# Performance work log

Measured on AMD Instinct MI355X. Metric: run time of the kernel, lower is better.

Reference implementation:

```python
import jax, jax.numpy as jnp
import numpy as np
from jax import lax

K = 5  # SCNN_KERNEL_LENGTH
PAD = K - 1
PAD_L = PAD // 2
PAD_R = PAD - PAD_L


def setup_inputs() -> dict:
    key = jax.random.key(0)
    k1, k2 = jax.random.split(key)
    B, H, W, C = 16, 256, 256, 32
    inputs = jax.random.normal(k1, (B, H, W, C), dtype=jnp.float32)
    # keras 'random_uniform' init is small; scale randn similarly to keep relu chain stable
    w = jax.random.normal(k2, (C, K, 1, C), dtype=jnp.float32) * 0.05
    b = jnp.zeros((C,), dtype=jnp.float32)
    return {"inputs": inputs, "w": w, "b": b}


def _mvcnn_down(inputs, w, b):
    # inputs: [B,H,W,C]; w: [C,K,1,C] (tf filter: [fh=C, fw=K, in=1, out=C])
    # The tf conv of the transposed row [B,C,W,1] with this filter is exactly a
    # 1D conv over W mixing all C input channels:
    #   out[b,x,o] = sum_{k,c} row_pad[b, x+k, c] * w[c,k,0,o]
    kernel = jnp.transpose(w[:, :, 0, :], (1, 0, 2))  # [K, C_in, C_out]

    def conv_row(x):  # x: [B,W,C] -> [B,W,C]
        return lax.conv_general_dilated(
            x, kernel, window_strides=(1,), padding=[(PAD_L, PAD_R)],
            dimension_numbers=("NWC", "WIO", "NWC"))

    rows = jnp.transpose(inputs, (1, 0, 2, 3))  # [H,B,W,C]

    def step(carry, row):
        # row i of the evolving state = original row + relu-conv result of row i-1
        x = row + carry
        r = jax.nn.relu(conv_row(x) + b)
        return r, r

    init = jnp.zeros_like(rows[0])
    _, out_rows = lax.scan(step, init, rows)  # [H,B,W,C]
    return jnp.transpose(out_rows, (1, 0, 2, 3))  # [B,H,W,C]


def reference(inputs, w, b):
    return _mvcnn_down(inputs, w, b)
```

## Files before the change

### kernel.cpp

```cpp
#include <hip/hip_runtime.h>
#include <stdint.h>

typedef _Float16 f16;
typedef _Float16 f16x2 __attribute__((ext_vector_type(2)));
typedef _Float16 f16x8 __attribute__((ext_vector_type(8)));
typedef float f32x4 __attribute__((ext_vector_type(4)));

#define NB 16
#define NH 256
#define NW 256
#define NC 32
#define NK 5

#define OWN 16
#define GC 16
#define NBLK (NB * GC)
#define XSTR 40
#define XROWS 36

#define FLAG_U32 16
#define NSLOT (NBLK * 2 * 2)
#define NFLAGS (NSLOT * FLAG_U32)
#define MAIL_BASE NFLAGS
#define MAIL_WORDS 128
#define KEYOF(k) (0x5EED0000u ^ (uint32_t)(k))

__device__ __forceinline__ void lds_barrier() {
  asm volatile("s_waitcnt lgkmcnt(0)\n\ts_barrier" ::: "memory");
}

__global__ __launch_bounds__(128, 1)
void mvcnn_down_mb(const float* __restrict__ in, const float* __restrict__ wt,
                   const float* __restrict__ bias, float* __restrict__ out,
                   uint32_t* __restrict__ ws) {
  __shared__ __align__(16) f16 xpad[2][XROWS * XSTR];

  const int bid  = blockIdx.x;
  const int b    = bid & 15;
  const int ck   = bid >> 4;
  const int t    = threadIdx.x;
  const int lane = t & 63;
  const int wv   = t >> 6;
  const int n16  = lane & 15;
  const int q    = lane >> 4;

  f16x8 bfrag[NK][2];
  #pragma unroll
  for (int tap = 0; tap < NK; ++tap) {
    #pragma unroll
    for (int nt = 0; nt < 2; ++nt) {
      f16x8 f;
      #pragma unroll
      for (int j = 0; j < 8; ++j) {
        int cch = q * 4 + (j >> 1) + (j & 1) * 16;
        f[j] = (f16)wt[(cch * NK + tap) * NC + nt * 16 + n16];
      }
      bfrag[tap][nt] = f;
    }
  }
  const float bias0 = bias[n16];
  const float bias1 = bias[16 + n16];

  for (int i = t; i < (int)(2 * XROWS * XSTR / 2); i += 128)
    ((uint32_t*)&xpad[0][0])[i] = 0u;

  const float* inb  = in  + (size_t)b * NH * NW * NC;
  float*       outb = out + (size_t)b * NH * NW * NC;

  const int lc0   = wv * 16 + q * 4;
  const int gcol0 = ck * 16 - 8 + lc0;

  int boff[4];
  #pragma unroll
  for (int r = 0; r < 4; ++r) {
    int g  = gcol0 + r;
    int gc = g < 0 ? 0 : (g > NW - 1 ? NW - 1 : g);
    boff[r] = (gc * NC + n16) * 4;
  }
  const bool ostore = wv ? (q < 2) : (q >= 2);
  const int  gown0  = wv ? (ck * 16 + 8 + q * 4) : (ck * 16 + (q - 2) * 4);

  uint32_t* flags = ws;
  uint32_t* mail  = ws + MAIL_BASE;
  const bool haspeer = wv ? (ck < GC - 1) : (ck > 0);
  const int  myslot2 = (bid * 2 + wv) * 2;
  const int  nbslot2 = wv ? ((bid + 16) * 2 + 0) * 2
                          : ((bid - 16) * 2 + 1) * 2;
  const int  smi     = wv ? (q * 4) * 16 : ((q - 2) * 4) * 16;

  float pf0[8], pf1[8];
  auto load_row = [&](int h1, float (&pf)[8]) {
    if (h1 >= NH) return;
    const char* rp = (const char*)(inb + (size_t)h1 * NW * NC);
    #pragma unroll
    for (int r = 0; r < 4; ++r) {
      pf[2 * r]     = *(const float*)(rp + boff[r]);
      pf[2 * r + 1] = *(const float*)(rp + boff[r] + 64);
    }
  };

  #pragma unroll
  for (int r = 0; r < 4; ++r) {
    int g = gcol0 + r;
    if ((unsigned)g < NW) {
      f16x2 v;
      v[0] = (f16)inb[g * NC + n16];
      v[1] = (f16)inb[g * NC + 16 + n16];
      *(f16x2*)(&xpad[0][(lc0 + r + 2) * XSTR + 2 * n16]) = v;
    }
  }
  load_row(1, pf0);
  load_row(2, pf1);
  __syncthreads();

  auto body = [&](const int h, float (&pf)[8], f16* xc, f16* xn,
                  bool recv, bool send) {
    if (recv) {
      const int k = h >> 2, ms = k & 1;
      if (haspeer) {
        if (lane == 0) {
          while (__hip_atomic_load(&flags[(nbslot2 + ms) * FLAG_U32],
                                   __ATOMIC_RELAXED, __HIP_MEMORY_SCOPE_AGENT)
                 != KEYOF(k))
            __builtin_amdgcn_s_sleep(2);
        }
        asm volatile("" ::: "memory");
        if (q < 2) {
          const uint32_t* mb = mail + (size_t)(nbslot2 + ms) * MAIL_WORDS;
          #pragma unroll
          for (int r = 0; r < 4; ++r) {
            uint32_t u = __hip_atomic_load(&mb[(q * 4 + r) * 16 + n16],
                                           __ATOMIC_RELAXED,
                                           __HIP_MEMORY_SCOPE_AGENT);
            const int lc = (wv ? 24 : 0) + q * 4 + r;
            *(uint32_t*)(&xc[(lc + 2) * XSTR + 2 * n16]) = u;
          }
        }
      }
    }

    f32x4 acc0 = {bias0, bias0, bias0, bias0};
    f32x4 acc1 = {bias1, bias1, bias1, bias1};
    #pragma unroll
    for (int tap = 0; tap < NK; ++tap) {
      f16x8 af = *(const f16x8*)(xc + (wv * 16 + n16 + tap) * XSTR + q * 8);
      acc0 = __builtin_amdgcn_mfma_f32_16x16x32_f16(af, bfrag[tap][0], acc0, 0, 0, 0);
      acc1 = __builtin_amdgcn_mfma_f32_16x16x32_f16(af, bfrag[tap][1], acc1, 0, 0, 0);
    }

    uint32_t sb[4] = {0, 0, 0, 0};
    float y0v[4], y1v[4];
    #pragma unroll
    for (int r = 0; r < 4; ++r) {
      float y0 = fmaxf(acc0[r], 0.f);
      float y1 = fmaxf(acc1[r], 0.f);
      y0v[r] = y0; y1v[r] = y1;
      int g = gcol0 + r;
      if (h < NH - 1 && (unsigned)g < NW) {
        f16x2 v;
        v[0] = (f16)(pf[2 * r]     + y0);
        v[1] = (f16)(pf[2 * r + 1] + y1);
        *(f16x2*)(&xn[(lc0 + r + 2) * XSTR + 2 * n16]) = v;
        sb[r] = __builtin_bit_cast(uint32_t, v);
      }
    }

    if (send && (h + 1) < NH) {
      const int k = (h + 1) >> 2, ms = k & 1;
      if (haspeer) {
        if (ostore) {
          uint32_t* mb = mail + (size_t)(myslot2 + ms) * MAIL_WORDS;
          #pragma unroll
          for (int r = 0; r < 4; ++r)
            __hip_atomic_store(&mb[smi + r * 16 + n16], sb[r],
                               __ATOMIC_RELAXED, __HIP_MEMORY_SCOPE_AGENT);
        }
        asm volatile("s_waitcnt vmcnt(0)" ::: "memory");
        if (lane == 0)
          __hip_atomic_store(&flags[(myslot2 + ms) * FLAG_U32], KEYOF(k),
                             __ATOMIC_RELAXED, __HIP_MEMORY_SCOPE_AGENT);
      }
    }

    if (ostore) {
      float* orow = outb + (size_t)h * NW * NC;
      #pragma unroll
      for (int r = 0; r < 4; ++r) {
        orow[(gown0 + r) * NC + n16]      = y0v[r];
        orow[(gown0 + r) * NC + 16 + n16] = y1v[r];
      }
    }

    load_row(h + 3, pf);
    lds_barrier();
  };

  f16* B0 = &xpad[0][0];
  f16* B1 = &xpad[1][0];
  for (int h4 = 0; h4 < NH; h4 += 4) {
    body(h4,     pf0, B0, B1, h4 > 0, false);
    body(h4 + 1, pf1, B1, B0, false,  false);
    body(h4 + 2, pf0, B0, B1, false,  false);
    body(h4 + 3, pf1, B1, B0, false,  true);
  }
}

__global__ __launch_bounds__(1024, 4)
void mvcnn_down(const float* __restrict__ in, const float* __restrict__ wt,
                const float* __restrict__ bias, float* __restrict__ out) {
  __shared__ __align__(16) f16 xpad[2][260 * XSTR];

  const int b    = blockIdx.x;
  const int t    = threadIdx.x;
  const int lane = t & 63;
  const int wv   = t >> 6;
  const int n16  = lane & 15;
  const int q    = lane >> 4;

  f16x8 bfrag[NK][2];
  #pragma unroll
  for (int tap = 0; tap < NK; ++tap) {
    #pragma unroll
    for (int nt = 0; nt < 2; ++nt) {
      f16x8 f;
      #pragma unroll
      for (int j = 0; j < 8; ++j) {
        int cch = q * 4 + (j >> 1) + (j & 1) * 16;
        f[j] = (f16)wt[(cch * NK + tap) * NC + nt * 16 + n16];
      }
      bfrag[tap][nt] = f;
    }
  }
  const float bias0 = bias[n16];
  const float bias1 = bias[16 + n16];

  for (int i = t; i < 2 * 260 * XSTR; i += 1024) (&xpad[0][0])[i] = (f16)0.f;
  __syncthreads();

  const float* inb  = in  + (size_t)b * NH * NW * NC;
  float*       outb = out + (size_t)b * NH * NW * NC;

  const int wo0  = wv * 16 + q * 4;
  const int arow = wv * 16 + n16;

  float pf0[8], pf1[8];
  auto load_in_row = [&](int h1, float (&pf)[8]) {
    const float* rp = inb + (size_t)h1 * NW * NC;
    #pragma unroll
    for (int r = 0; r < 4; ++r) {
      int wo = wo0 + r;
      pf[2 * r]     = rp[wo * NC + n16];
      pf[2 * r + 1] = rp[wo * NC + 16 + n16];
    }
  };

  #pragma unroll
  for (int r = 0; r < 4; ++r) {
    int wo = wo0 + r;
    f16x2 v;
    v[0] = (f16)inb[wo * NC + n16];
    v[1] = (f16)inb[wo * NC + 16 + n16];
    *(f16x2*)(&xpad[0][(wo + 2) * XSTR + 2 * n16]) = v;
  }
  load_in_row(1, pf0);
  load_in_row(2, pf1);
  __syncthreads();

  auto body = [&](const int h, float (&pf)[8], const f16* xp_cur, f16* xp_nxt) {
    f32x4 acc0 = {0.f, 0.f, 0.f, 0.f};
    f32x4 acc1 = {0.f, 0.f, 0.f, 0.f};
    #pragma unroll
    for (int tap = 0; tap < NK; ++tap) {
      f16x8 af = *(const f16x8*)(xp_cur + (arow + tap) * XSTR + q * 8);
      acc0 = __builtin_amdgcn_mfma_f32_16x16x32_f16(af, bfrag[tap][0], acc0, 0, 0, 0);
      acc1 = __builtin_amdgcn_mfma_f32_16x16x32_f16(af, bfrag[tap][1], acc1, 0, 0, 0);
    }
    float* orow = outb + (size_t)h * NW * NC;
    #pragma unroll
    for (int r = 0; r < 4; ++r) {
      float y0 = acc0[r] + bias0; y0 = y0 > 0.f ? y0 : 0.f;
      float y1 = acc1[r] + bias1; y1 = y1 > 0.f ? y1 : 0.f;
      int wo = wo0 + r;
      orow[wo * NC + n16]      = y0;
      orow[wo * NC + 16 + n16] = y1;
      if (h < NH - 1) {
        f16x2 v;
        v[0] = (f16)(pf[2 * r]     + y0);
        v[1] = (f16)(pf[2 * r + 1] + y1);
        *(f16x2*)(&xp_nxt[(wo + 2) * XSTR + 2 * n16]) = v;
      }
    }
    if (h + 3 < NH) load_in_row(h + 3, pf);
    lds_barrier();
  };

  const f16* xA = &xpad[0][0];
  f16* xB = &xpad[1][0];
  for (int h = 0; h < NH; h += 2) {
    body(h,     pf0, xA, xB);
    body(h + 1, pf1, xB, (f16*)xA);
  }
}

extern "C" void kernel_launch(void* const* d_in, const int* in_sizes, int n_in,
                              void* d_out, int out_size, void* d_ws, size_t ws_size,
                              hipStream_t stream) {
  const float* in   = (const float*)d_in[0];
  const float* wt   = (const float*)d_in[1];
  const float* bias = (const float*)d_in[2];
  float* out = (float*)d_out;

  const size_t need = (size_t)(NFLAGS + NSLOT * MAIL_WORDS) * 4;
  if (d_ws != nullptr && ws_size >= need) {
    hipLaunchKernelGGL(mvcnn_down_mb, dim3(NBLK), dim3(128), 0, stream,
                       in, wt, bias, out, (uint32_t*)d_ws);
  } else {
    hipLaunchKernelGGL(mvcnn_down, dim3(NB), dim3(1024), 0, stream,
                       in, wt, bias, out);
  }
}
```

Measured before the change: 428.5 us.

## Widen halo to 16 columns per side and exchange every 8 rows

Each block now runs three waves: a middle wave computes the 16 owned columns, and two side waves recompute 16-column halos on either side, instead of two waves with 8-column halos. The middle wave publishes its owned row to a mailbox, and neighbours read it only every 8 rows instead of every 4. This halves the number of cross-block flag handshakes and spin waits, which are meant to be the serialising cost of the 256-step recurrence. In exchange it adds redundant halo computation and global loads per row, and grows the LDS tile and mailbox size.

Result: faster. 408.7 us (-4.6%).

```diff
diff --git a/kernel.cpp b/kernel.cpp
--- a/kernel.cpp
+++ b/kernel.cpp
@@ -16,20 +16,19 @@
 #define GC 16
 #define NBLK (NB * GC)
 #define XSTR 40
-#define XROWS 36
+#define XROWS 52
 
 #define FLAG_U32 16
-#define NSLOT (NBLK * 2 * 2)
-#define NFLAGS (NSLOT * FLAG_U32)
+#define NFLAGS (NBLK * 2 * FLAG_U32)
 #define MAIL_BASE NFLAGS
-#define MAIL_WORDS 128
+#define MAIL_WORDS 256
 #define KEYOF(k) (0x5EED0000u ^ (uint32_t)(k))
 
 __device__ __forceinline__ void lds_barrier() {
   asm volatile("s_waitcnt lgkmcnt(0)\n\ts_barrier" ::: "memory");
 }
 
-__global__ __launch_bounds__(128, 1)
+__global__ __launch_bounds__(192, 1)
 void mvcnn_down_mb(const float* __restrict__ in, const float* __restrict__ wt,
                    const float* __restrict__ bias, float* __restrict__ out,
                    uint32_t* __restrict__ ws) {
@@ -44,6 +43,8 @@
   const int n16  = lane & 15;
   const int q    = lane >> 4;
 
+  const bool act = (wv == 1) || (wv == 0 ? (ck > 0) : (ck < GC - 1));
+
   f16x8 bfrag[NK][2];
   #pragma unroll
   for (int tap = 0; tap < NK; ++tap) {
@@ -61,36 +62,34 @@
   const float bias0 = bias[n16];
   const float bias1 = bias[16 + n16];
 
-  for (int i = t; i < (int)(2 * XROWS * XSTR / 2); i += 128)
+  for (int i = t; i < (int)(2 * XROWS * XSTR / 2); i += 192)
     ((uint32_t*)&xpad[0][0])[i] = 0u;
+  __syncthreads();
 
   const float* inb  = in  + (size_t)b * NH * NW * NC;
   float*       outb = out + (size_t)b * NH * NW * NC;
 
-  const int lc0   = wv * 16 + q * 4;
-  const int gcol0 = ck * 16 - 8 + lc0;
+  const int wo0  = wv * 16 + q * 4;
+  const int arow = wv * 16 + n16;
 
   int boff[4];
   #pragma unroll
   for (int r = 0; r < 4; ++r) {
-    int g  = gcol0 + r;
-    int gc = g < 0 ? 0 : (g > NW - 1 ? NW - 1 : g);
-    boff[r] = (gc * NC + n16) * 4;
-  }
-  const bool ostore = wv ? (q < 2) : (q >= 2);
-  const int  gown0  = wv ? (ck * 16 + 8 + q * 4) : (ck * 16 + (q - 2) * 4);
+    int g = ck * OWN - 16 + wo0 + r;
+    boff[r] = ((g < 0 ? 0 : g) * NC + n16) * 4;
+  }
+  int ooff[4];
+  #pragma unroll
+  for (int r = 0; r < 4; ++r)
+    ooff[r] = ((ck * OWN + q * 4 + r) * NC + n16) * 4;
 
   uint32_t* flags = ws;
   uint32_t* mail  = ws + MAIL_BASE;
-  const bool haspeer = wv ? (ck < GC - 1) : (ck > 0);
-  const int  myslot2 = (bid * 2 + wv) * 2;
-  const int  nbslot2 = wv ? ((bid + 16) * 2 + 0) * 2
-                          : ((bid - 16) * 2 + 1) * 2;
-  const int  smi     = wv ? (q * 4) * 16 : ((q - 2) * 4) * 16;
+  const int midx  = (q * 4) * 16 + n16;
 
   float pf0[8], pf1[8];
   auto load_row = [&](int h1, float (&pf)[8]) {
-    if (h1 >= NH) return;
+    if (!act || h1 >= NH) return;
     const char* rp = (const char*)(inb + (size_t)h1 * NW * NC);
     #pragma unroll
     for (int r = 0; r < 4; ++r) {
@@ -99,51 +98,25 @@
     }
   };
 
-  #pragma unroll
-  for (int r = 0; r < 4; ++r) {
-    int g = gcol0 + r;
-    if ((unsigned)g < NW) {
+  if (act) {
+    #pragma unroll
+    for (int r = 0; r < 4; ++r) {
       f16x2 v;
-      v[0] = (f16)inb[g * NC + n16];
-      v[1] = (f16)inb[g * NC + 16 + n16];
-      *(f16x2*)(&xpad[0][(lc0 + r + 2) * XSTR + 2 * n16]) = v;
+      v[0] = (f16)*(const float*)((const char*)inb + boff[r]);
+      v[1] = (f16)*(const float*)((const char*)inb + boff[r] + 64);
+      *(f16x2*)(&xpad[0][(wo0 + r + 2) * XSTR + 2 * n16]) = v;
     }
   }
   load_row(1, pf0);
   load_row(2, pf1);
   __syncthreads();
 
-  auto body = [&](const int h, float (&pf)[8], f16* xc, f16* xn,
-                  bool recv, bool send) {
-    if (recv) {
-      const int k = h >> 2, ms = k & 1;
-      if (haspeer) {
-        if (lane == 0) {
-          while (__hip_atomic_load(&flags[(nbslot2 + ms) * FLAG_U32],
-                                   __ATOMIC_RELAXED, __HIP_MEMORY_SCOPE_AGENT)
-                 != KEYOF(k))
-            __builtin_amdgcn_s_sleep(2);
-        }
-        asm volatile("" ::: "memory");
-        if (q < 2) {
-          const uint32_t* mb = mail + (size_t)(nbslot2 + ms) * MAIL_WORDS;
-          #pragma unroll
-          for (int r = 0; r < 4; ++r) {
-            uint32_t u = __hip_atomic_load(&mb[(q * 4 + r) * 16 + n16],
-                                           __ATOMIC_RELAXED,
-                                           __HIP_MEMORY_SCOPE_AGENT);
-            const int lc = (wv ? 24 : 0) + q * 4 + r;
-            *(uint32_t*)(&xc[(lc + 2) * XSTR + 2 * n16]) = u;
-          }
-        }
-      }
-    }
-
+  auto body = [&](const int h, float (&pf)[8], f16* xc, f16* xn) {
     f32x4 acc0 = {bias0, bias0, bias0, bias0};
     f32x4 acc1 = {bias1, bias1, bias1, bias1};
     #pragma unroll
     for (int tap = 0; tap < NK; ++tap) {
-      f16x8 af = *(const f16x8*)(xc + (wv * 16 + n16 + tap) * XSTR + q * 8);
+      f16x8 af = *(const f16x8*)(xc + (arow + tap) * XSTR + q * 8);
       acc0 = __builtin_amdgcn_mfma_f32_16x16x32_f16(af, bfrag[tap][0], acc0, 0, 0, 0);
       acc1 = __builtin_amdgcn_mfma_f32_16x16x32_f16(af, bfrag[tap][1], acc1, 0, 0, 0);
     }
@@ -155,39 +128,54 @@
       float y0 = fmaxf(acc0[r], 0.f);
       float y1 = fmaxf(acc1[r], 0.f);
       y0v[r] = y0; y1v[r] = y1;
-      int g = gcol0 + r;
-      if (h < NH - 1 && (unsigned)g < NW) {
+      if (h < NH - 1 && act) {
         f16x2 v;
         v[0] = (f16)(pf[2 * r]     + y0);
         v[1] = (f16)(pf[2 * r + 1] + y1);
-        *(f16x2*)(&xn[(lc0 + r + 2) * XSTR + 2 * n16]) = v;
+        *(f16x2*)(&xn[(wo0 + r + 2) * XSTR + 2 * n16]) = v;
         sb[r] = __builtin_bit_cast(uint32_t, v);
       }
     }
 
-    if (send && (h + 1) < NH) {
-      const int k = (h + 1) >> 2, ms = k & 1;
-      if (haspeer) {
-        if (ostore) {
-          uint32_t* mb = mail + (size_t)(myslot2 + ms) * MAIL_WORDS;
-          #pragma unroll
-          for (int r = 0; r < 4; ++r)
-            __hip_atomic_store(&mb[smi + r * 16 + n16], sb[r],
-                               __ATOMIC_RELAXED, __HIP_MEMORY_SCOPE_AGENT);
-        }
+    if (((h + 1) & 7) == 0 && (h + 1) < NH) {
+      const int k  = (h + 1) >> 3;
+      const int ms = k & 1;
+      if (wv == 1) {
+        uint32_t* mb = mail + ((size_t)(bid * 2 + ms)) * MAIL_WORDS;
+        #pragma unroll
+        for (int r = 0; r < 4; ++r)
+          __hip_atomic_store(&mb[midx + r * 16], sb[r],
+                             __ATOMIC_RELAXED, __HIP_MEMORY_SCOPE_AGENT);
         asm volatile("s_waitcnt vmcnt(0)" ::: "memory");
         if (lane == 0)
-          __hip_atomic_store(&flags[(myslot2 + ms) * FLAG_U32], KEYOF(k),
+          __hip_atomic_store(&flags[(bid * 2 + ms) * FLAG_U32], KEYOF(k),
                              __ATOMIC_RELAXED, __HIP_MEMORY_SCOPE_AGENT);
-      }
-    }
-
-    if (ostore) {
-      float* orow = outb + (size_t)h * NW * NC;
+      } else if (act) {
+        const int nbid = (wv == 0) ? (bid - 16) : (bid + 16);
+        if (lane == 0) {
+          while (__hip_atomic_load(&flags[(nbid * 2 + ms) * FLAG_U32],
+                                   __ATOMIC_RELAXED, __HIP_MEMORY_SCOPE_AGENT)
+                 != KEYOF(k))
+            __builtin_amdgcn_s_sleep(1);
+        }
+        asm volatile("" ::: "memory");
+        const uint32_t* mb = mail + ((size_t)(nbid * 2 + ms)) * MAIL_WORDS;
+        #pragma unroll
+        for (int r = 0; r < 4; ++r) {
+          uint32_t u = __hip_atomic_load(&mb[midx + r * 16],
+                                         __ATOMIC_RELAXED,
+                                         __HIP_MEMORY_SCOPE_AGENT);
+          *(uint32_t*)(&xn[(wo0 + r + 2) * XSTR + 2 * n16]) = u;
+        }
+      }
+    }
+
+    if (wv == 1) {
+      char* orow = (char*)outb + (size_t)h * (NW * NC * 4);
       #pragma unroll
       for (int r = 0; r < 4; ++r) {
-        orow[(gown0 + r) * NC + n16]      = y0v[r];
-        orow[(gown0 + r) * NC + 16 + n16] = y1v[r];
+        *(float*)(orow + ooff[r])      = y0v[r];
+        *(float*)(orow + ooff[r] + 64) = y1v[r];
       }
     }
 
@@ -197,11 +185,9 @@
 
   f16* B0 = &xpad[0][0];
   f16* B1 = &xpad[1][0];
-  for (int h4 = 0; h4 < NH; h4 += 4) {
-    body(h4,     pf0, B0, B1, h4 > 0, false);
-    body(h4 + 1, pf1, B1, B0, false,  false);
-    body(h4 + 2, pf0, B0, B1, false,  false);
-    body(h4 + 3, pf1, B1, B0, false,  true);
+  for (int h = 0; h < NH; h += 2) {
+    body(h,     pf0, B0, B1);
+    body(h + 1, pf1, B1, B0);
   }
 }
 
@@ -310,9 +296,9 @@
   const float* bias = (const float*)d_in[2];
   float* out = (float*)d_out;
 
-  const size_t need = (size_t)(NFLAGS + NSLOT * MAIL_WORDS) * 4;
+  const size_t need = (size_t)(NFLAGS + NBLK * 2 * MAIL_WORDS) * 4;
   if (d_ws != nullptr && ws_size >= need) {
-    hipLaunchKernelGGL(mvcnn_down_mb, dim3(NBLK), dim3(128), 0, stream,
+    hipLaunchKernelGGL(mvcnn_down_mb, dim3(NBLK), dim3(192), 0, stream,
                        in, wt, bias, out, (uint32_t*)d_ws);
   } else {
     hipLaunchKernelGGL(mvcnn_down, dim3(NB), dim3(1024), 0, stream,
```
